# Kernel optimization log

Hardware: AMD Instinct MI355X
Metric: run time of the kernel (lower is better)

Reference implementation:

```python
import jax, jax.numpy as jnp
import numpy as np

B, S, D, H = 4, 2048, 1024, 16
HD = D // H

def setup_inputs() -> dict:
    key = jax.random.key(0)
    ks = jax.random.split(key, 9)
    s = 1.0 / np.sqrt(D)
    return {
        "x": jax.random.normal(ks[0], (B, S, D), dtype=jnp.float32),
        "wq": jax.random.uniform(ks[1], (D, D), jnp.float32, -s, s),
        "bq": jnp.zeros((D,), jnp.float32),
        "wk": jax.random.uniform(ks[2], (D, D), jnp.float32, -s, s),
        "bk": jnp.zeros((D,), jnp.float32),
        "wv": jax.random.uniform(ks[3], (D, D), jnp.float32, -s, s),
        "bv": jnp.zeros((D,), jnp.float32),
        "wo": jax.random.uniform(ks[4], (D, D), jnp.float32, -s, s),
        "bo": jnp.zeros((D,), jnp.float32),
    }

def reference(x, wq, bq, wk, bk, wv, bv, wo, bo):
    b, s, _ = x.shape
    # project and split heads: [B,S,D] -> [B,H,S,HD]
    def heads(w, bias):
        return (x @ w.T + bias).reshape(b, s, H, HD).transpose(0, 2, 1, 3)
    q = heads(wq, bq)
    k = heads(wk, bk)
    v = heads(wv, bv)
    scale = 1.0 / jnp.sqrt(jnp.float32(HD))
    scores = jnp.einsum("bhqd,bhkd->bhqk", q, k) * scale
    attn = jax.nn.softmax(scores, axis=-1)
    out = jnp.einsum("bhqk,bhkd->bhqd", attn, v)
    out = out.transpose(0, 2, 1, 3).reshape(b, s, D)
    return out @ wo.T + bo
```

## Files before the change

### kernel.cpp

```cpp
#include <hip/hip_runtime.h>
#include <stdint.h>


#define B_ 4
#define S_ 2048
#define D_ 1024
#define H_ 16
#define HD_ 64
#define M_ (B_ * S_)

typedef __bf16 bf16x8 __attribute__((ext_vector_type(8)));
typedef float f32x4 __attribute__((ext_vector_type(4)));
typedef float f32x16 __attribute__((ext_vector_type(16)));
typedef unsigned short u16;

#define QSCALE 0.18033688011112042f
#define THR2 11.0f

__device__ __forceinline__ u16 f2bf(float f) {
  union { float f; unsigned u; } v; v.f = f;
  unsigned u = v.u;
  u += 0x7fff + ((u >> 16) & 1);
  return (u16)(u >> 16);
}

__device__ __forceinline__ float exp2_fast(float x) {
#if __has_builtin(__builtin_amdgcn_exp2f)
  return __builtin_amdgcn_exp2f(x);
#else
  return __expf(x * 0.69314718056f);
#endif
}

__device__ __forceinline__ unsigned packbf(float a, float b) {
  union { unsigned u; __bf16 h[2]; } v;
  v.h[0] = (__bf16)a; v.h[1] = (__bf16)b;
  return v.u;
}

__device__ __forceinline__ void gl2lds16(const void* g, void* l) {
  __builtin_amdgcn_global_load_lds(
      (const __attribute__((address_space(1))) unsigned int*)g,
      (__attribute__((address_space(3))) unsigned int*)l, 16, 0, 0);
}

__global__ __launch_bounds__(256) void convert_kernel(
    const float* __restrict__ x, const float* __restrict__ wq,
    const float* __restrict__ wk, const float* __restrict__ wv,
    const float* __restrict__ wo, u16* __restrict__ xb, u16* __restrict__ wqb,
    u16* __restrict__ wkb, u16* __restrict__ wvb, u16* __restrict__ wob) {
  const int64_t NX = (int64_t)M_ * D_ / 4;
  const int64_t NW = (int64_t)D_ * D_ / 4;
  int64_t i = (int64_t)blockIdx.x * blockDim.x + threadIdx.x;
  const float* src; u16* dst; int64_t off;
  if (i < NX)              { src = x;  dst = xb;  off = i; }
  else if (i < NX + NW)    { src = wq; dst = wqb; off = i - NX; }
  else if (i < NX + 2*NW)  { src = wk; dst = wkb; off = i - NX - NW; }
  else if (i < NX + 3*NW)  { src = wv; dst = wvb; off = i - NX - 2*NW; }
  else                     { src = wo; dst = wob; off = i - NX - 3*NW; }
  float4 v = reinterpret_cast<const float4*>(src)[off];
  ushort4 o;
  o.x = f2bf(v.x); o.y = f2bf(v.y); o.z = f2bf(v.z); o.w = f2bf(v.w);
  reinterpret_cast<ushort4*>(dst)[off] = o;
}

template <int MODE>
__global__ __launch_bounds__(256) void gemm_kernel(
    const u16* __restrict__ A, const u16* __restrict__ Bw,
    const float* __restrict__ bias, void* __restrict__ out) {
  __shared__ u16 As[128 * 64];
  __shared__ u16 Bs[128 * 64];
  const int tid = threadIdx.x;
  const int lane = tid & 63;
  const int wid = tid >> 6;
  const int row0 = blockIdx.y * 128;
  const int col0 = blockIdx.x * 128;
  const int wr = (wid >> 1) * 64;
  const int wc = (wid & 1) * 64;

  f32x4 acc[4][4] = {};
  const int srow = lane >> 3;
  const int cc = (lane & 7) ^ srow;

  for (int kt = 0; kt < D_; kt += 64) {
    __syncthreads();
    for (int t = 0; t < 4; ++t) {
      int r = (wid * 4 + t) * 8 + srow;
      gl2lds16(A + (int64_t)(row0 + r) * D_ + kt + cc * 8,
               (char*)As + (wid * 4 + t) * 1024);
      gl2lds16(Bw + (int64_t)(col0 + r) * D_ + kt + cc * 8,
               (char*)Bs + (wid * 4 + t) * 1024);
    }
    __syncthreads();

    bf16x8 af[4][2], bfr[4][2];
#pragma unroll
    for (int mi = 0; mi < 4; ++mi)
#pragma unroll
      for (int ks = 0; ks < 2; ++ks) {
        int c = ks * 4 + (lane >> 4);
        int ra = wr + mi * 16 + (lane & 15);
        af[mi][ks] = *reinterpret_cast<const bf16x8*>(
            (char*)As + ra * 128 + ((c ^ (ra & 7)) << 4));
        int rb = wc + mi * 16 + (lane & 15);
        bfr[mi][ks] = *reinterpret_cast<const bf16x8*>(
            (char*)Bs + rb * 128 + ((c ^ (rb & 7)) << 4));
      }
#pragma unroll
    for (int ks = 0; ks < 2; ++ks)
#pragma unroll
      for (int mi = 0; mi < 4; ++mi)
#pragma unroll
        for (int ni = 0; ni < 4; ++ni) {
          if (MODE == 1)
            acc[mi][ni] = __builtin_amdgcn_mfma_f32_16x16x32_bf16(
                bfr[ni][ks], af[mi][ks], acc[mi][ni], 0, 0, 0);
          else
            acc[mi][ni] = __builtin_amdgcn_mfma_f32_16x16x32_bf16(
                af[mi][ks], bfr[ni][ks], acc[mi][ni], 0, 0, 0);
        }
  }

  if (MODE == 0 || MODE == 3) {
    u16* o = (u16*)out;
#pragma unroll
    for (int mi = 0; mi < 4; ++mi)
#pragma unroll
      for (int ni = 0; ni < 4; ++ni) {
        int j = col0 + wc + ni * 16 + (lane & 15);
        float bvv = bias[j];
        int h = j >> 6, hd = j & 63;
#pragma unroll
        for (int r = 0; r < 4; ++r) {
          int i = row0 + wr + mi * 16 + (lane >> 4) * 4 + r;
          int b = i >> 11, s = i & 2047;
          float val = acc[mi][ni][r] + bvv;
          if (MODE == 3) val *= QSCALE;
          o[((int64_t)(b * H_ + h) * S_ + s) * HD_ + hd] = f2bf(val);
        }
      }
  } else if (MODE == 1) {
    u16* o = (u16*)out;
#pragma unroll
    for (int mi = 0; mi < 4; ++mi)
#pragma unroll
      for (int ni = 0; ni < 4; ++ni) {
        int i = row0 + wr + mi * 16 + (lane & 15);
        int b = i >> 11, s = i & 2047;
#pragma unroll
        for (int r = 0; r < 4; ++r) {
          int j = col0 + wc + ni * 16 + (lane >> 4) * 4 + r;
          int h = j >> 6, hd = j & 63;
          o[((int64_t)(b * H_ + h) * HD_ + hd) * S_ + s] = f2bf(acc[mi][ni][r] + bias[j]);
        }
      }
  } else {
    float* o = (float*)out;
#pragma unroll
    for (int mi = 0; mi < 4; ++mi)
#pragma unroll
      for (int ni = 0; ni < 4; ++ni) {
        int j = col0 + wc + ni * 16 + (lane & 15);
        float bvv = bias[j];
#pragma unroll
        for (int r = 0; r < 4; ++r) {
          int i = row0 + wr + mi * 16 + (lane >> 4) * 4 + r;
          o[(int64_t)i * D_ + j] = acc[mi][ni][r] + bvv;
        }
      }
  }
}

__global__ __launch_bounds__(512, 2) void attn_kernel(
    const u16* __restrict__ Q, const u16* __restrict__ Kg,
    const u16* __restrict__ Vt, u16* __restrict__ AO) {
  __shared__ u16 Ks[2][64 * 64];
  __shared__ u16 Vs[2][64 * 64];
  const int tid = threadIdx.x;
  const int lane = tid & 63;
  const int l31 = lane & 31;
  const int hi = lane >> 5;
  const int wid = tid >> 6;
  const int orig = blockIdx.x;
  const int swz = (orig & 7) * 32 + (orig >> 3);
  const int bh = swz >> 2;
  const int qw = (swz & 3) * 512 + wid * 64;

  bf16x8 qf[2][4];
#pragma unroll
  for (int qb = 0; qb < 2; ++qb)
#pragma unroll
    for (int ks = 0; ks < 4; ++ks)
      qf[qb][ks] = *reinterpret_cast<const bf16x8*>(
          Q + ((int64_t)bh * S_ + qw + qb * 32 + l31) * HD_ + ks * 16 + hi * 8);

  bf16x8 ones8;
#pragma unroll
  for (int i = 0; i < 8; ++i) ones8[i] = (__bf16)1.0f;

  f32x16 o0[2] = {}, o1[2] = {}, ls[2] = {};
  float mrow[2] = {-1e30f, -1e30f};

  const int srow = lane >> 3;
  const int cc = (lane & 7) ^ srow;

  const u16* kp = Kg + ((int64_t)bh * S_ + wid * 8 + srow) * HD_ + cc * 8;
  const u16* vp = Vt + ((int64_t)bh * HD_ + wid * 8 + srow) * S_ + cc * 8;

  gl2lds16(kp, (char*)Ks[0] + wid * 1024); kp += 64 * HD_;
  gl2lds16(vp, (char*)Vs[0] + wid * 1024); vp += 64;

  const int NT = S_ / 64;

#define TILE_STEP(T, CUR)                                                      \
  {                                                                            \
    asm volatile("s_waitcnt vmcnt(0)" ::: "memory");                           \
    __builtin_amdgcn_s_barrier();                                              \
    if ((T) + 1 < NT) {                                                        \
      gl2lds16(kp, (char*)Ks[(CUR) ^ 1] + wid * 1024);                         \
      gl2lds16(vp, (char*)Vs[(CUR) ^ 1] + wid * 1024);                         \
      kp += 64 * HD_; vp += 64;                                                \
    }                                                                          \
    f32x16 sc0[2] = {{}, {}}, sc1[2] = {{}, {}};                               \
    {                                                                          \
      const char* kbase = (const char*)Ks[CUR];                                \
      __builtin_amdgcn_s_setprio(1);                                           \
      _Pragma("unroll")                                                        \
      for (int ks = 0; ks < 4; ++ks) {                                         \
        int chunk = 2 * ks + hi;                                               \
        int r0 = l31, r1 = 32 + l31;                                           \
        bf16x8 k0 = *reinterpret_cast<const bf16x8*>(                          \
            kbase + r0 * 128 + ((chunk ^ (r0 & 7)) << 4));                     \
        bf16x8 k1 = *reinterpret_cast<const bf16x8*>(                          \
            kbase + r1 * 128 + ((chunk ^ (r1 & 7)) << 4));                     \
        _Pragma("unroll")                                                      \
        for (int qb = 0; qb < 2; ++qb) {                                       \
          sc0[qb] = __builtin_amdgcn_mfma_f32_32x32x16_bf16(k0, qf[qb][ks],    \
                                                            sc0[qb], 0, 0, 0); \
          sc1[qb] = __builtin_amdgcn_mfma_f32_32x32x16_bf16(k1, qf[qb][ks],    \
                                                            sc1[qb], 0, 0, 0); \
        }                                                                      \
      }                                                                        \
      __builtin_amdgcn_s_setprio(0);                                           \
    }                                                                          \
    float mx[2];                                                               \
    _Pragma("unroll")                                                          \
    for (int qb = 0; qb < 2; ++qb) {                                           \
      float a8[8];                                                             \
      _Pragma("unroll")                                                        \
      for (int i = 0; i < 8; ++i)                                              \
        a8[i] = fmaxf(fmaxf(fmaxf(sc0[qb][2 * i], sc0[qb][2 * i + 1]),         \
                            sc1[qb][2 * i]), sc1[qb][2 * i + 1]);              \
      mx[qb] = fmaxf(fmaxf(fmaxf(fmaxf(a8[0], a8[1]), a8[2]), a8[3]),          \
                     fmaxf(fmaxf(fmaxf(a8[4], a8[5]), a8[6]), a8[7]));         \
    }                                                                          \
    int okd = (mx[0] - mrow[0] <= THR2 && mx[1] - mrow[1] <= THR2) ? 1 : 0;    \
    if (!__all(okd)) {                                                         \
      _Pragma("unroll")                                                        \
      for (int qb = 0; qb < 2; ++qb) {                                         \
        float mxf = fmaxf(mx[qb], __shfl_xor(mx[qb], 32));                     \
        float mnew = fmaxf(mrow[qb], mxf);                                     \
        float al = exp2_fast(mrow[qb] - mnew);                                 \
        mrow[qb] = mnew;                                                       \
        _Pragma("unroll")                                                      \
        for (int tt = 0; tt < 16; ++tt) {                                      \
          float at = __shfl(al, (tt & 3) + 8 * (tt >> 2) + 4 * hi);            \
          o0[qb][tt] *= at; o1[qb][tt] *= at; ls[qb][tt] *= at;                \
        }                                                                      \
      }                                                                        \
    }                                                                          \
    unsigned w[2][2][4][2], rv[2][2][2][2];                                    \
    _Pragma("unroll")                                                          \
    for (int qb = 0; qb < 2; ++qb) {                                           \
      _Pragma("unroll")                                                        \
      for (int tt = 0; tt < 16; ++tt) {                                        \
        sc0[qb][tt] = exp2_fast(sc0[qb][tt] - mrow[qb]);                       \
        sc1[qb][tt] = exp2_fast(sc1[qb][tt] - mrow[qb]);                       \
      }                                                                        \
      _Pragma("unroll")                                                        \
      for (int rr = 0; rr < 4; ++rr) {                                         \
        w[qb][0][rr][0] = packbf(sc0[qb][4 * rr], sc0[qb][4 * rr + 1]);        \
        w[qb][0][rr][1] = packbf(sc0[qb][4 * rr + 2], sc0[qb][4 * rr + 3]);    \
        w[qb][1][rr][0] = packbf(sc1[qb][4 * rr], sc1[qb][4 * rr + 1]);        \
        w[qb][1][rr][1] = packbf(sc1[qb][4 * rr + 2], sc1[qb][4 * rr + 3]);    \
      }                                                                        \
      _Pragma("unroll")                                                        \
      for (int n2 = 0; n2 < 2; ++n2) {                                         \
        _Pragma("unroll")                                                      \
        for (int c = 0; c < 2; ++c) {                                          \
          _Pragma("unroll")                                                    \
          for (int h2 = 0; h2 < 2; ++h2)                                       \
            rv[qb][n2][c][h2] = (unsigned)__shfl_xor(                          \
                (int)(hi ? w[qb][n2][2 * c][h2] : w[qb][n2][2 * c + 1][h2]),   \
                32);                                                           \
        }                                                                      \
      }                                                                        \
    }                                                                          \
    {                                                                          \
      const char* vbase = (const char*)Vs[CUR];                                \
      __builtin_amdgcn_s_setprio(1);                                           \
      _Pragma("unroll")                                                        \
      for (int kb = 0; kb < 4; ++kb) {                                         \
        const int c = kb & 1, n2 = kb >> 1;                                    \
        int chunk = 2 * kb + hi;                                               \
        int r0 = l31, r1 = 32 + l31;                                           \
        bf16x8 v0 = *reinterpret_cast<const bf16x8*>(                          \
            vbase + r0 * 128 + ((chunk ^ (r0 & 7)) << 4));                     \
        bf16x8 v1 = *reinterpret_cast<const bf16x8*>(                          \
            vbase + r1 * 128 + ((chunk ^ (r1 & 7)) << 4));                     \
        _Pragma("unroll")                                                      \
        for (int qb = 0; qb < 2; ++qb) {                                       \
          union { bf16x8 v; unsigned u[4]; } pu;                               \
          pu.u[0] = hi ? rv[qb][n2][c][0] : w[qb][n2][2 * c][0];               \
          pu.u[1] = hi ? rv[qb][n2][c][1] : w[qb][n2][2 * c][1];               \
          pu.u[2] = hi ? w[qb][n2][2 * c + 1][0] : rv[qb][n2][c][0];           \
          pu.u[3] = hi ? w[qb][n2][2 * c + 1][1] : rv[qb][n2][c][1];           \
          o0[qb] = __builtin_amdgcn_mfma_f32_32x32x16_bf16(pu.v, v0, o0[qb],   \
                                                           0, 0, 0);           \
          o1[qb] = __builtin_amdgcn_mfma_f32_32x32x16_bf16(pu.v, v1, o1[qb],   \
                                                           0, 0, 0);           \
          ls[qb] = __builtin_amdgcn_mfma_f32_32x32x16_bf16(pu.v, ones8,        \
                                                           ls[qb], 0, 0, 0);   \
        }                                                                      \
      }                                                                        \
      __builtin_amdgcn_s_setprio(0);                                           \
    }                                                                          \
  }

  for (int t = 0; t < NT; t += 2) {
    TILE_STEP(t, 0)
    TILE_STEP(t + 1, 1)
  }
#undef TILE_STEP

  const int b = bh >> 4, h = bh & 15;
#pragma unroll
  for (int qb = 0; qb < 2; ++qb)
#pragma unroll
    for (int tt = 0; tt < 16; ++tt) {
      int row = (tt & 3) + 8 * (tt >> 2) + 4 * hi;
      float inv = __builtin_amdgcn_rcpf(ls[qb][tt]);
      int qr = qw + qb * 32 + row;
      int64_t base = ((int64_t)(b * S_ + qr)) * D_ + h * HD_ + l31;
      AO[base] = f2bf(o0[qb][tt] * inv);
      AO[base + 32] = f2bf(o1[qb][tt] * inv);
    }
}

extern "C" void kernel_launch(void* const* d_in, const int* in_sizes, int n_in,
                              void* d_out, int out_size, void* d_ws, size_t ws_size,
                              hipStream_t stream) {
  const float* x  = (const float*)d_in[0];
  const float* wq = (const float*)d_in[1];
  const float* bq = (const float*)d_in[2];
  const float* wk = (const float*)d_in[3];
  const float* bk = (const float*)d_in[4];
  const float* wv = (const float*)d_in[5];
  const float* bv = (const float*)d_in[6];
  const float* wo = (const float*)d_in[7];
  const float* bo = (const float*)d_in[8];
  char* ws = (char*)d_ws;
  u16* xb  = (u16*)ws;
  u16* wqb = (u16*)(ws + (16ll << 20));
  u16* wkb = (u16*)(ws + (18ll << 20));
  u16* wvb = (u16*)(ws + (20ll << 20));
  u16* wob = (u16*)(ws + (22ll << 20));
  u16* q   = (u16*)(ws + (24ll << 20));
  u16* k   = (u16*)(ws + (40ll << 20));
  u16* vt  = (u16*)(ws + (56ll << 20));
  u16* ao  = xb;

  convert_kernel<<<12288, 256, 0, stream>>>(x, wq, wk, wv, wo, xb, wqb, wkb, wvb, wob);
  dim3 gg(D_ / 128, M_ / 128);
  gemm_kernel<3><<<gg, 256, 0, stream>>>(xb, wqb, bq, q);
  gemm_kernel<0><<<gg, 256, 0, stream>>>(xb, wkb, bk, k);
  gemm_kernel<1><<<gg, 256, 0, stream>>>(xb, wvb, bv, vt);
  attn_kernel<<<256, 512, 0, stream>>>(q, k, vt, ao);
  gemm_kernel<2><<<gg, 256, 0, stream>>>(ao, wob, bo, (float*)d_out);
}
```

Before: 224.3 us.

## Permute K tile rows so P registers feed PV MFMA without cross-lane shuffles

Key rows are loaded into LDS in a permuted order (bits 2 and 3 of the row index swapped). With that order, the score accumulator layout of the QK MFMA lines up directly with the A-operand layout the PV MFMA expects. This removes the __shfl_xor exchanges and per-lane selects that rebuilt P fragments on every tile. Softmax is invariant to key order as long as V stays in its natural order, so correctness depends on that permutation mapping exactly.

```diff
diff --git a/kernel.cpp b/kernel.cpp
--- a/kernel.cpp
+++ b/kernel.cpp
@@ -13,6 +13,7 @@
 typedef float f32x4 __attribute__((ext_vector_type(4)));
 typedef float f32x16 __attribute__((ext_vector_type(16)));
 typedef unsigned short u16;
+typedef union { bf16x8 v; unsigned u[4]; } bfu;
 
 #define QSCALE 0.18033688011112042f
 #define THR2 11.0f
@@ -204,8 +205,10 @@
   const int srow = lane >> 3;
   const int cc = (lane & 7) ^ srow;
 
-  const u16* kp = Kg + ((int64_t)bh * S_ + wid * 8 + srow) * HD_ + cc * 8;
-  const u16* vp = Vt + ((int64_t)bh * HD_ + wid * 8 + srow) * S_ + cc * 8;
+  const int lr = wid * 8 + srow;
+  const int sr = (lr & ~12) | ((lr & 4) << 1) | ((lr & 8) >> 1);
+  const u16* kp = Kg + ((int64_t)bh * S_ + sr) * HD_ + cc * 8;
+  const u16* vp = Vt + ((int64_t)bh * HD_ + lr) * S_ + cc * 8;
 
   gl2lds16(kp, (char*)Ks[0] + wid * 1024); kp += 64 * HD_;
   gl2lds16(vp, (char*)Vs[0] + wid * 1024); vp += 64;
@@ -269,7 +272,7 @@
         }                                                                      \
       }                                                                        \
     }                                                                          \
-    unsigned w[2][2][4][2], rv[2][2][2][2];                                    \
+    bfu pa[2][4];                                                              \
     _Pragma("unroll")                                                          \
     for (int qb = 0; qb < 2; ++qb) {                                           \
       _Pragma("unroll")                                                        \
@@ -278,22 +281,11 @@
         sc1[qb][tt] = exp2_fast(sc1[qb][tt] - mrow[qb]);                       \
       }                                                                        \
       _Pragma("unroll")                                                        \
-      for (int rr = 0; rr < 4; ++rr) {                                         \
-        w[qb][0][rr][0] = packbf(sc0[qb][4 * rr], sc0[qb][4 * rr + 1]);        \
-        w[qb][0][rr][1] = packbf(sc0[qb][4 * rr + 2], sc0[qb][4 * rr + 3]);    \
-        w[qb][1][rr][0] = packbf(sc1[qb][4 * rr], sc1[qb][4 * rr + 1]);        \
-        w[qb][1][rr][1] = packbf(sc1[qb][4 * rr + 2], sc1[qb][4 * rr + 3]);    \
-      }                                                                        \
-      _Pragma("unroll")                                                        \
-      for (int n2 = 0; n2 < 2; ++n2) {                                         \
-        _Pragma("unroll")                                                      \
-        for (int c = 0; c < 2; ++c) {                                          \
-          _Pragma("unroll")                                                    \
-          for (int h2 = 0; h2 < 2; ++h2)                                       \
-            rv[qb][n2][c][h2] = (unsigned)__shfl_xor(                          \
-                (int)(hi ? w[qb][n2][2 * c][h2] : w[qb][n2][2 * c + 1][h2]),   \
-                32);                                                           \
-        }                                                                      \
+      for (int m = 0; m < 4; ++m) {                                            \
+        pa[qb][0].u[m] = packbf(sc0[qb][2 * m], sc0[qb][2 * m + 1]);           \
+        pa[qb][1].u[m] = packbf(sc0[qb][8 + 2 * m], sc0[qb][9 + 2 * m]);       \
+        pa[qb][2].u[m] = packbf(sc1[qb][2 * m], sc1[qb][2 * m + 1]);           \
+        pa[qb][3].u[m] = packbf(sc1[qb][8 + 2 * m], sc1[qb][9 + 2 * m]);       \
       }                                                                        \
     }                                                                          \
     {                                                                          \
@@ -301,7 +293,6 @@
       __builtin_amdgcn_s_setprio(1);                                           \
       _Pragma("unroll")                                                        \
       for (int kb = 0; kb < 4; ++kb) {                                         \
-        const int c = kb & 1, n2 = kb >> 1;                                    \
         int chunk = 2 * kb + hi;                                               \
         int r0 = l31, r1 = 32 + l31;                                           \
         bf16x8 v0 = *reinterpret_cast<const bf16x8*>(                          \
@@ -310,17 +301,13 @@
             vbase + r1 * 128 + ((chunk ^ (r1 & 7)) << 4));                     \
         _Pragma("unroll")                                                      \
         for (int qb = 0; qb < 2; ++qb) {                                       \
-          union { bf16x8 v; unsigned u[4]; } pu;                               \
-          pu.u[0] = hi ? rv[qb][n2][c][0] : w[qb][n2][2 * c][0];               \
-          pu.u[1] = hi ? rv[qb][n2][c][1] : w[qb][n2][2 * c][1];               \
-          pu.u[2] = hi ? w[qb][n2][2 * c + 1][0] : rv[qb][n2][c][0];           \
-          pu.u[3] = hi ? w[qb][n2][2 * c + 1][1] : rv[qb][n2][c][1];           \
-          o0[qb] = __builtin_amdgcn_mfma_f32_32x32x16_bf16(pu.v, v0, o0[qb],   \
+          o0[qb] = __builtin_amdgcn_mfma_f32_32x32x16_bf16(pa[qb][kb].v, v0,   \
+                                                           o0[qb], 0, 0, 0);   \
+          o1[qb] = __builtin_amdgcn_mfma_f32_32x32x16_bf16(pa[qb][kb].v, v1,   \
+                                                           o1[qb], 0, 0, 0);   \
+          ls[qb] = __builtin_amdgcn_mfma_f32_32x32x16_bf16(pa[qb][kb].v,       \
+                                                           ones8, ls[qb],      \
                                                            0, 0, 0);           \
-          o1[qb] = __builtin_amdgcn_mfma_f32_32x32x16_bf16(pu.v, v1, o1[qb],   \
-                                                           0, 0, 0);           \
-          ls[qb] = __builtin_amdgcn_mfma_f32_32x32x16_bf16(pu.v, ones8,        \
-                                                           ls[qb], 0, 0, 0);   \
         }                                                                      \
       }                                                                        \
       __builtin_amdgcn_s_setprio(0);                                           \
```

After: 217.6 us. 1.03x faster.
